# Kernel optimization log

Hardware: AMD Instinct MI355X
Metric: run time of the kernel (lower is better)

Reference implementation:

```python
import jax, jax.numpy as jnp
import numpy as np

DIM = 512
N_HEAD = 4
WIN = (5, 9)

def setup_inputs() -> dict:
    key = jax.random.key(0)
    ks = jax.random.split(key, 9)
    s = DIM ** -0.5
    x = jax.random.normal(ks[0], (1, 8, 60, 108, DIM), jnp.float32)
    Wq = jax.random.normal(ks[1], (DIM, DIM), jnp.float32) * s
    bq = jax.random.normal(ks[2], (DIM,), jnp.float32) * 0.02
    Wk = jax.random.normal(ks[3], (DIM, DIM), jnp.float32) * s
    bk = jax.random.normal(ks[4], (DIM,), jnp.float32) * 0.02
    Wv = jax.random.normal(ks[5], (DIM, DIM), jnp.float32) * s
    bv = jax.random.normal(ks[6], (DIM,), jnp.float32) * 0.02
    Wp = jax.random.normal(ks[7], (DIM, DIM), jnp.float32) * s
    bp = jax.random.normal(ks[8], (DIM,), jnp.float32) * 0.02
    return {"x": x, "Wq": Wq, "bq": bq, "Wk": Wk, "bk": bk,
            "Wv": Wv, "bv": bv, "Wp": Wp, "bp": bp}

def reference(x, Wq, bq, Wk, bk, Wv, bv, Wp, bp):
    b, t, h, w, c = x.shape
    w_h, w_w = WIN
    n_head = N_HEAD
    c_head = c // n_head
    n_wh = -(-h // w_h)
    n_ww = -(-w // w_w)
    new_h, new_w = n_wh * w_h, n_ww * w_w
    pad_b, pad_r = new_h - h, new_w - w
    if pad_b > 0 or pad_r > 0:
        x = jnp.pad(x, ((0, 0), (0, 0), (0, pad_b), (0, pad_r), (0, 0)))
    # torch nn.Linear: y = x @ W.T + b, weight shape (out, in)
    q = jnp.einsum('bthwc,dc->bthwd', x, Wq) + bq
    k = jnp.einsum('bthwc,dc->bthwd', x, Wk) + bk
    v = jnp.einsum('bthwc,dc->bthwd', x, Wv) + bv

    def part(z):
        # (b,t,H,W,c) -> (b, n_windows, n_head, t*w_h*w_w, c_head)
        z = z.reshape(b, t, n_wh, w_h, n_ww, w_w, n_head, c_head)
        z = z.transpose(0, 2, 4, 6, 1, 3, 5, 7)
        return z.reshape(b, n_wh * n_ww, n_head, t * w_h * w_w, c_head)

    qw, kw, vw = part(q), part(k), part(v)
    scale = c_head ** -0.5
    # all (batch, window) attentions batched into one einsum (fused form of the torch double loop)
    scores = jnp.einsum('bwnsc,bwnkc->bwnsk', qw, kw) * scale
    attn = jax.nn.softmax(scores, axis=-1)
    out = jnp.einsum('bwnsk,bwnkc->bwnsc', attn, vw)
    # merge windows back: (b,t,new_h,new_w,c)
    out = out.reshape(b, n_wh, n_ww, n_head, t, w_h, w_w, c_head)
    out = out.transpose(0, 4, 1, 5, 2, 6, 3, 7).reshape(b, t, new_h, new_w, c)
    out = out[:, :, :h, :w, :]
    out = jnp.einsum('bthwc,dc->bthwd', out, Wp) + bp
    return out
```

## Files before the change

kernel.cpp:

```cpp
#include <hip/hip_runtime.h>

typedef _Float16 f16;
typedef _Float16 f16x8 __attribute__((ext_vector_type(8)));
typedef _Float16 f16x4 __attribute__((ext_vector_type(4)));
typedef float f32x4 __attribute__((ext_vector_type(4)));
typedef unsigned int u32;
typedef unsigned int u32x4 __attribute__((ext_vector_type(4)));

#define MFMA16(a, b, c) __builtin_amdgcn_mfma_f32_16x16x32_f16(a, b, c, 0, 0, 0)

__device__ __forceinline__ void async_copy16(f16* lds, const f16* g) {
    __builtin_amdgcn_global_load_lds(
        (const __attribute__((address_space(1))) unsigned int*)g,
        (__attribute__((address_space(3))) unsigned int*)lds,
        16, 0, 0);
}

__global__ __launch_bounds__(256) void prep_convert(
    const float* __restrict__ x, f16* __restrict__ xh,
    const float* __restrict__ Wq, const float* __restrict__ Wk,
    const float* __restrict__ Wv, const float* __restrict__ Wp,
    const float* __restrict__ bq, const float* __restrict__ bk,
    const float* __restrict__ bv,
    f16* __restrict__ Wqkv, f16* __restrict__ Wph, float* __restrict__ bqkv,
    int* __restrict__ tokmap)
{
    if (blockIdx.x < 12960) {
        int i = blockIdx.x * 256 + threadIdx.x;
        f32x4 a = *(const f32x4*)(x + (size_t)i * 8);
        f32x4 b = *(const f32x4*)(x + (size_t)i * 8 + 4);
        f16x8 h = { (f16)a[0], (f16)a[1], (f16)a[2], (f16)a[3],
                    (f16)b[0], (f16)b[1], (f16)b[2], (f16)b[3] };
        *(f16x8*)(xh + (size_t)i * 8) = h;
        return;
    }
    int i = (blockIdx.x - 12960) * 256 + threadIdx.x;
    if (i < 786432) {
        int r = i >> 9, c = i & 511;
        const float* src = (r < 512) ? Wq : (r < 1024) ? Wk : Wv;
        Wqkv[i] = (f16)src[(r & 511) * 512 + c];
    } else if (i < 786432 + 262144) {
        int j = i - 786432;
        Wph[j] = (f16)Wp[j];
    } else if (i < 786432 + 262144 + 1536) {
        int j = i - (786432 + 262144);
        bqkv[j] = (j < 512) ? bq[j] : (j < 1024) ? bk[j - 512] : bv[j - 1024];
    } else if (i < 786432 + 262144 + 1536 + 51840) {
        int j = i - (786432 + 262144 + 1536);
        int t_ = j / 6480, rem = j % 6480;
        int hh = rem / 108, ww = rem % 108;
        int win = (hh / 5) * 12 + (ww / 9);
        int s = t_ * 45 + (hh % 5) * 9 + (ww % 9);
        tokmap[j] = win * 1440 + s;
    }
}

__global__ __launch_bounds__(256, 3) void qkv_gemm(
    const f16* __restrict__ Xh, const f16* __restrict__ W,
    const float* __restrict__ bias, const int* __restrict__ tokmap,
    f16* __restrict__ Qp, f16* __restrict__ Kp, f16* __restrict__ Vp)
{
    __shared__ __align__(16) f16 As[3][128 * 32];
    __shared__ __align__(16) f16 Bs[3][128 * 32];
    const int tid = threadIdx.x;
    const int lane = tid & 63, wid = tid >> 6;
    const int g = lane >> 4, l15 = lane & 15;
    const int wr = wid >> 1, wc = wid & 1;

    const int orig = blockIdx.x;
    const int xcd = orig & 7;
    const int wg = (xcd < 4 ? xcd * 608 : 2432 + (xcd - 4) * 607) + (orig >> 3);
    const int bn = wg % 12;
    const int brow = (wg / 12) * 128;

    const f16* Abase = Xh + (size_t)brow * 512;
    const f16* Bbase = W + (size_t)bn * 128 * 512;

    f32x4 acc[4][4] = {};

    #define QKV_STAGE(buf, step)                                              \
        {                                                                     \
            const int k0_ = (step) * 32;                                      \
            _Pragma("unroll")                                                 \
            for (int rr = 0; rr < 2; ++rr) {                                  \
                int idx = rr * 256 + tid;                                     \
                int row = idx >> 2, ch = idx & 3;                             \
                int sch = ch ^ ((row >> 1) & 3);                              \
                async_copy16(&As[buf][idx * 8],                               \
                             Abase + (size_t)row * 512 + k0_ + sch * 8);      \
                async_copy16(&Bs[buf][idx * 8],                               \
                             Bbase + (size_t)row * 512 + k0_ + sch * 8);      \
            }                                                                 \
        }

    QKV_STAGE(0, 0);
    QKV_STAGE(1, 1);

    int cur = 0;
    for (int t = 0; t < 16; ++t) {
        if (t < 15) asm volatile("s_waitcnt vmcnt(4)" ::: "memory");
        else        asm volatile("s_waitcnt vmcnt(0)" ::: "memory");
        __builtin_amdgcn_s_barrier();
        __builtin_amdgcn_sched_barrier(0);
        if (t + 2 < 16) {
            int stg = cur + 2; if (stg >= 3) stg -= 3;
            QKV_STAGE(stg, t + 2);
        }
        f16x8 a[4], b[4];
        #pragma unroll
        for (int m = 0; m < 4; ++m) {
            int arow = wr * 64 + m * 16 + l15;
            int sl = g ^ ((arow >> 1) & 3);
            a[m] = *(const f16x8*)&As[cur][arow * 32 + sl * 8];
        }
        #pragma unroll
        for (int n = 0; n < 4; ++n) {
            int brw = wc * 64 + n * 16 + l15;
            int sl = g ^ ((brw >> 1) & 3);
            b[n] = *(const f16x8*)&Bs[cur][brw * 32 + sl * 8];
        }
        __builtin_amdgcn_s_setprio(1);
        #pragma unroll
        for (int m = 0; m < 4; ++m)
            #pragma unroll
            for (int n = 0; n < 4; ++n)
                acc[m][n] = MFMA16(a[m], b[n], acc[m][n]);
        __builtin_amdgcn_s_setprio(0);
        __builtin_amdgcn_s_barrier();
        cur = (cur == 2) ? 0 : cur + 1;
    }
    #undef QKV_STAGE

    const int which = bn >> 2, head = bn & 3;
    f16* dst = (which == 0) ? Qp : (which == 1) ? Kp : Vp;
    #pragma unroll
    for (int m = 0; m < 4; ++m) {
        #pragma unroll
        for (int j = 0; j < 4; ++j) {
            int gm = brow + wr * 64 + m * 16 + g * 4 + j;
            size_t obase = ((size_t)(tokmap[gm] + head * 360)) * 128;
            #pragma unroll
            for (int n = 0; n < 4; ++n) {
                int cidx = wc * 64 + n * 16 + l15;
                float v = acc[m][n][j] + bias[bn * 128 + cidx];
                dst[obase + cidx] = (f16)v;
            }
        }
    }
}

__global__ __launch_bounds__(256, 2) void attn_kernel(
    const f16* __restrict__ Qp, const f16* __restrict__ Kp,
    const f16* __restrict__ Vp, f16* __restrict__ AO)
{
    __shared__ __align__(128) f16 Kl[2][64 * 128];
    __shared__ __align__(16)  f16 Vt[128 * 76];
    __shared__ __align__(16)  f16 Pl[192 * 68];

    const int tid = threadIdx.x;
    const int lane = tid & 63, wid = tid >> 6;
    const int g = lane >> 4, l15 = lane & 15;
    const int orig = blockIdx.x;
    const int bid = (orig & 7) * 144 + (orig >> 3);
    const int wh = bid >> 1;
    const int half = bid & 1;
    const int win = wh >> 2, head = wh & 3;
    const int base = wh * 46080;
    const int qbase = half * 192 + wid * 48;

    const float SC2 = 0.08838834764831845f * 1.4426950408889634f;

    #define STAGE_K(buf, kt_)                                                 \
        {                                                                     \
            _Pragma("unroll")                                                 \
            for (int it = 0; it < 4; ++it) {                                  \
                int chunk = it * 256 + tid;                                   \
                int krow = chunk >> 4, c = chunk & 15;                        \
                int sc_ = c ^ (krow & 7);                                     \
                async_copy16(&Kl[buf][chunk * 8],                             \
                    Kp + base + (size_t)((kt_) * 64 + krow) * 128 + sc_ * 8); \
            }                                                                 \
        }

    f16x8 qf[3][4];
    #pragma unroll
    for (int qi = 0; qi < 3; ++qi)
        #pragma unroll
        for (int c4 = 0; c4 < 4; ++c4)
            qf[qi][c4] = *(const f16x8*)(Qp + base + (qbase + qi * 16 + l15) * 128 + c4 * 32 + g * 8);

    STAGE_K(0, 0);

    f32x4 o[3][8] = {};
    float l_r[3] = { 0.f, 0.f, 0.f };

    for (int kt = 0; kt < 6; ++kt) {
        const int cb = kt & 1;
        #pragma unroll
        for (int it = 0; it < 2; ++it) {
            int i2 = it * 256 + tid;
            int kb = i2 >> 6;
            int chp = (i2 & 63) * 2;
            const u32* Vb = (const u32*)(Vp + base);
            u32 d[8];
            #pragma unroll
            for (int i = 0; i < 8; ++i) {
                int kg = kt * 64 + kb * 8 + i;
                d[i] = (kg < 360) ? Vb[kg * 64 + (chp >> 1)] : 0u;
            }
            u32x4 lo, hi;
            #pragma unroll
            for (int jj = 0; jj < 4; ++jj) {
                lo[jj] = (d[2 * jj] & 0xffffu) | (d[2 * jj + 1] << 16);
                hi[jj] = (d[2 * jj] >> 16) | (d[2 * jj + 1] & 0xffff0000u);
            }
            *(u32x4*)&Vt[chp * 76 + kb * 8] = lo;
            *(u32x4*)&Vt[(chp + 1) * 76 + kb * 8] = hi;
        }
        __syncthreads();
        if (kt + 1 < 6) STAGE_K(cb ^ 1, kt + 1);

        f32x4 sc[4][3] = {};
        __builtin_amdgcn_s_setprio(1);
        #pragma unroll
        for (int c4 = 0; c4 < 4; ++c4) {
            f16x8 ka[4];
            #pragma unroll
            for (int kf = 0; kf < 4; ++kf) {
                int row = kf * 16 + l15;
                int sl = (c4 * 4 + g) ^ (row & 7);
                ka[kf] = *(const f16x8*)&Kl[cb][row * 128 + sl * 8];
            }
            #pragma unroll
            for (int kf = 0; kf < 4; ++kf)
                #pragma unroll
                for (int qi = 0; qi < 3; ++qi)
                    sc[kf][qi] = MFMA16(ka[kf], qf[qi][c4], sc[kf][qi]);
        }
        __builtin_amdgcn_s_setprio(0);
        if (kt == 5) {
            #pragma unroll
            for (int kf = 0; kf < 4; ++kf)
                #pragma unroll
                for (int j = 0; j < 4; ++j)
                    if (320 + kf * 16 + g * 4 + j >= 360) {
                        #pragma unroll
                        for (int qi = 0; qi < 3; ++qi) sc[kf][qi][j] = -1e30f;
                    }
        }

        #pragma unroll
        for (int qi = 0; qi < 3; ++qi) {
            float psum = 0.f;
            #pragma unroll
            for (int kf = 0; kf < 4; ++kf) {
                f16x4 pv;
                #pragma unroll
                for (int j = 0; j < 4; ++j) {
                    float p = exp2f(sc[kf][qi][j] * SC2);
                    psum += p;
                    pv[j] = (f16)p;
                }
                *(f16x4*)&Pl[(wid * 48 + qi * 16 + l15) * 68 + kf * 16 + g * 4] = pv;
            }
            psum += __shfl_xor(psum, 16);
            psum += __shfl_xor(psum, 32);
            l_r[qi] += psum;
        }

        __builtin_amdgcn_s_setprio(1);
        #pragma unroll
        for (int kc = 0; kc < 2; ++kc) {
            f16x8 pa[3], vb[8];
            #pragma unroll
            for (int qi = 0; qi < 3; ++qi)
                pa[qi] = *(const f16x8*)&Pl[(wid * 48 + qi * 16 + l15) * 68 + kc * 32 + g * 8];
            #pragma unroll
            for (int chf = 0; chf < 8; ++chf)
                vb[chf] = *(const f16x8*)&Vt[(chf * 16 + l15) * 76 + kc * 32 + g * 8];
            #pragma unroll
            for (int qi = 0; qi < 3; ++qi)
                #pragma unroll
                for (int chf = 0; chf < 8; ++chf)
                    o[qi][chf] = MFMA16(pa[qi], vb[chf], o[qi][chf]);
        }
        __builtin_amdgcn_s_setprio(0);
        __syncthreads();
    }
    #undef STAGE_K

    #pragma unroll
    for (int qi = 0; qi < 3; ++qi) {
        #pragma unroll
        for (int j = 0; j < 4; ++j) {
            float lj = __shfl(l_r[qi], g * 4 + j);
            float inv = 1.0f / lj;
            int s = qbase + qi * 16 + g * 4 + j;
            if (s < 360) {
                int t_ = s / 45, s45 = s % 45;
                int hh = (win / 12) * 5 + s45 / 9;
                int ww = (win % 12) * 9 + s45 % 9;
                int mm = t_ * 6480 + hh * 108 + ww;
                #pragma unroll
                for (int chf = 0; chf < 8; ++chf) {
                    int col = head * 128 + chf * 16 + l15;
                    AO[(size_t)mm * 512 + col] = (f16)(o[qi][chf][j] * inv);
                }
            }
        }
    }
}

__global__ __launch_bounds__(256, 3) void proj_gemm(
    const f16* __restrict__ A, const f16* __restrict__ W,
    const float* __restrict__ bias, float* __restrict__ out)
{
    __shared__ __align__(16) f16 As[3][128 * 32];
    __shared__ __align__(16) f16 Bs[3][128 * 32];
    const int tid = threadIdx.x;
    const int lane = tid & 63, wid = tid >> 6;
    const int g = lane >> 4, l15 = lane & 15;
    const int wr = wid >> 1, wc = wid & 1;

    const int orig = blockIdx.x;
    const int xcd = orig & 7;
    const int wg = (xcd < 4 ? xcd * 203 : 812 + (xcd - 4) * 202) + (orig >> 3);
    const int bcol = (wg & 3) * 128;
    const int brow = (wg >> 2) * 128;

    const f16* Abase = A + (size_t)brow * 512;
    const f16* Bbase = W + (size_t)bcol * 512;

    f32x4 acc[4][4] = {};

    #define PROJ_STAGE(buf, step)                                             \
        {                                                                     \
            const int k0_ = (step) * 32;                                      \
            _Pragma("unroll")                                                 \
            for (int rr = 0; rr < 2; ++rr) {                                  \
                int idx = rr * 256 + tid;                                     \
                int row = idx >> 2, ch = idx & 3;                             \
                int sch = ch ^ ((row >> 1) & 3);                              \
                async_copy16(&As[buf][idx * 8],                               \
                             Abase + (size_t)row * 512 + k0_ + sch * 8);      \
                async_copy16(&Bs[buf][idx * 8],                               \
                             Bbase + (size_t)row * 512 + k0_ + sch * 8);      \
            }                                                                 \
        }

    PROJ_STAGE(0, 0);
    PROJ_STAGE(1, 1);

    int cur = 0;
    for (int t = 0; t < 16; ++t) {
        if (t < 15) asm volatile("s_waitcnt vmcnt(4)" ::: "memory");
        else        asm volatile("s_waitcnt vmcnt(0)" ::: "memory");
        __builtin_amdgcn_s_barrier();
        __builtin_amdgcn_sched_barrier(0);
        if (t + 2 < 16) {
            int stg = cur + 2; if (stg >= 3) stg -= 3;
            PROJ_STAGE(stg, t + 2);
        }
        f16x8 a[4], b[4];
        #pragma unroll
        for (int m = 0; m < 4; ++m) {
            int arow = wr * 64 + m * 16 + l15;
            int sl = g ^ ((arow >> 1) & 3);
            a[m] = *(const f16x8*)&As[cur][arow * 32 + sl * 8];
        }
        #pragma unroll
        for (int n = 0; n < 4; ++n) {
            int brw = wc * 64 + n * 16 + l15;
            int sl = g ^ ((brw >> 1) & 3);
            b[n] = *(const f16x8*)&Bs[cur][brw * 32 + sl * 8];
        }
        __builtin_amdgcn_s_setprio(1);
        #pragma unroll
        for (int m = 0; m < 4; ++m)
            #pragma unroll
            for (int n = 0; n < 4; ++n)
                acc[m][n] = MFMA16(a[m], b[n], acc[m][n]);
        __builtin_amdgcn_s_setprio(0);
        __builtin_amdgcn_s_barrier();
        cur = (cur == 2) ? 0 : cur + 1;
    }
    #undef PROJ_STAGE

    #pragma unroll
    for (int m = 0; m < 4; ++m)
        #pragma unroll
        for (int j = 0; j < 4; ++j) {
            int gm = brow + wr * 64 + m * 16 + g * 4 + j;
            #pragma unroll
            for (int n = 0; n < 4; ++n) {
                int gn = bcol + wc * 64 + n * 16 + l15;
                out[(size_t)gm * 512 + gn] = acc[m][n][j] + bias[gn];
            }
        }
}

extern "C" void kernel_launch(void* const* d_in, const int* in_sizes, int n_in,
                              void* d_out, int out_size, void* d_ws, size_t ws_size,
                              hipStream_t stream)
{
    (void)in_sizes; (void)n_in; (void)out_size; (void)ws_size;
    const float* x  = (const float*)d_in[0];
    const float* Wq = (const float*)d_in[1];
    const float* bq = (const float*)d_in[2];
    const float* Wk = (const float*)d_in[3];
    const float* bk = (const float*)d_in[4];
    const float* Wv = (const float*)d_in[5];
    const float* bv = (const float*)d_in[6];
    const float* Wp = (const float*)d_in[7];
    const float* bp = (const float*)d_in[8];

    f16* Qp   = (f16*)d_ws;
    f16* Kp   = Qp + 26542080;
    f16* Vp   = Kp + 26542080;
    f16* AO   = Vp + 26542080;
    f16* xh   = AO;
    f16* Wqkv = AO + 26542080;
    f16* Wph  = Wqkv + 786432;
    float* bqkv = (float*)(Wph + 262144);
    int* tokmap = (int*)(bqkv + 1536);

    prep_convert<<<17265, 256, 0, stream>>>(x, xh, Wq, Wk, Wv, Wp, bq, bk, bv,
                                            Wqkv, Wph, bqkv, tokmap);
    qkv_gemm<<<4860, 256, 0, stream>>>(xh, Wqkv, bqkv, tokmap, Qp, Kp, Vp);
    attn_kernel<<<1152, 256, 0, stream>>>(Qp, Kp, Vp, AO);
    proj_gemm<<<1620, 256, 0, stream>>>(AO, Wph, bp, (float*)d_out);
}
```

Baseline: 262.3 us.

## Fuse fp32-to-fp16 activation conversion into QKV GEMM with register-staged A loads

Removes the separate pass that converted x to fp16 in a workspace buffer. The QKV GEMM now reads fp32 x directly into registers, converts to fp16 and writes it swizzled into LDS, while B keeps using async global-to-LDS copies. The main loop is restructured into a register double-buffered pipeline with explicit waitcnt/barrier placement. This saves a full write and read of the fp16 copy, but each GEMM block now reads fp32 A 12 times across the N tiles, and register pressure rises.

Result: slower. 305.5 us (+16.5%).

```diff
diff --git a/kernel.cpp b/kernel.cpp
--- a/kernel.cpp
+++ b/kernel.cpp
@@ -16,8 +16,7 @@
         16, 0, 0);
 }
 
-__global__ __launch_bounds__(256) void prep_convert(
-    const float* __restrict__ x, f16* __restrict__ xh,
+__global__ __launch_bounds__(256) void prep_kernel(
     const float* __restrict__ Wq, const float* __restrict__ Wk,
     const float* __restrict__ Wv, const float* __restrict__ Wp,
     const float* __restrict__ bq, const float* __restrict__ bk,
@@ -25,16 +24,7 @@
     f16* __restrict__ Wqkv, f16* __restrict__ Wph, float* __restrict__ bqkv,
     int* __restrict__ tokmap)
 {
-    if (blockIdx.x < 12960) {
-        int i = blockIdx.x * 256 + threadIdx.x;
-        f32x4 a = *(const f32x4*)(x + (size_t)i * 8);
-        f32x4 b = *(const f32x4*)(x + (size_t)i * 8 + 4);
-        f16x8 h = { (f16)a[0], (f16)a[1], (f16)a[2], (f16)a[3],
-                    (f16)b[0], (f16)b[1], (f16)b[2], (f16)b[3] };
-        *(f16x8*)(xh + (size_t)i * 8) = h;
-        return;
-    }
-    int i = (blockIdx.x - 12960) * 256 + threadIdx.x;
+    int i = blockIdx.x * 256 + threadIdx.x;
     if (i < 786432) {
         int r = i >> 9, c = i & 511;
         const float* src = (r < 512) ? Wq : (r < 1024) ? Wk : Wv;
@@ -56,7 +46,7 @@
 }
 
 __global__ __launch_bounds__(256, 3) void qkv_gemm(
-    const f16* __restrict__ Xh, const f16* __restrict__ W,
+    const float* __restrict__ X, const f16* __restrict__ W,
     const float* __restrict__ bias, const int* __restrict__ tokmap,
     f16* __restrict__ Qp, f16* __restrict__ Kp, f16* __restrict__ Vp)
 {
@@ -73,12 +63,37 @@
     const int bn = wg % 12;
     const int brow = (wg / 12) * 128;
 
-    const f16* Abase = Xh + (size_t)brow * 512;
+    const float* Abase = X + (size_t)brow * 512;
     const f16* Bbase = W + (size_t)bn * 128 * 512;
 
     f32x4 acc[4][4] = {};
-
-    #define QKV_STAGE(buf, step)                                              \
+    f32x4 arA[4], arB[4];
+
+    #define LOAD_A(bank, step)                                                \
+        {                                                                     \
+            _Pragma("unroll")                                                 \
+            for (int rr = 0; rr < 4; ++rr) {                                  \
+                int idx = rr * 256 + tid;                                     \
+                int row = idx >> 3, s = idx & 7;                              \
+                bank[rr] = *(const f32x4*)(Abase + (size_t)row * 512 +        \
+                                           (step) * 32 + s * 4);              \
+            }                                                                 \
+        }
+
+    #define CVT_WRITE(bank, step)                                             \
+        {                                                                     \
+            _Pragma("unroll")                                                 \
+            for (int rr = 0; rr < 4; ++rr) {                                  \
+                int idx = rr * 256 + tid;                                     \
+                int row = idx >> 3, s = idx & 7;                              \
+                int ws = (s >> 1) ^ ((row >> 1) & 3);                         \
+                f32x4 v = bank[rr];                                           \
+                f16x4 h = { (f16)v[0], (f16)v[1], (f16)v[2], (f16)v[3] };     \
+                *(f16x4*)&As[(step) % 3][row * 32 + ws * 8 + (s & 1) * 4] = h;\
+            }                                                                 \
+        }
+
+    #define LOAD_B(step)                                                      \
         {                                                                     \
             const int k0_ = (step) * 32;                                      \
             _Pragma("unroll")                                                 \
@@ -86,50 +101,58 @@
                 int idx = rr * 256 + tid;                                     \
                 int row = idx >> 2, ch = idx & 3;                             \
                 int sch = ch ^ ((row >> 1) & 3);                              \
-                async_copy16(&As[buf][idx * 8],                               \
-                             Abase + (size_t)row * 512 + k0_ + sch * 8);      \
-                async_copy16(&Bs[buf][idx * 8],                               \
+                async_copy16(&Bs[(step) % 3][idx * 8],                        \
                              Bbase + (size_t)row * 512 + k0_ + sch * 8);      \
             }                                                                 \
         }
 
-    QKV_STAGE(0, 0);
-    QKV_STAGE(1, 1);
-
-    int cur = 0;
-    for (int t = 0; t < 16; ++t) {
-        if (t < 15) asm volatile("s_waitcnt vmcnt(4)" ::: "memory");
-        else        asm volatile("s_waitcnt vmcnt(0)" ::: "memory");
-        __builtin_amdgcn_s_barrier();
-        __builtin_amdgcn_sched_barrier(0);
-        if (t + 2 < 16) {
-            int stg = cur + 2; if (stg >= 3) stg -= 3;
-            QKV_STAGE(stg, t + 2);
-        }
-        f16x8 a[4], b[4];
-        #pragma unroll
-        for (int m = 0; m < 4; ++m) {
-            int arow = wr * 64 + m * 16 + l15;
-            int sl = g ^ ((arow >> 1) & 3);
-            a[m] = *(const f16x8*)&As[cur][arow * 32 + sl * 8];
-        }
-        #pragma unroll
-        for (int n = 0; n < 4; ++n) {
-            int brw = wc * 64 + n * 16 + l15;
-            int sl = g ^ ((brw >> 1) & 3);
-            b[n] = *(const f16x8*)&Bs[cur][brw * 32 + sl * 8];
-        }
-        __builtin_amdgcn_s_setprio(1);
-        #pragma unroll
-        for (int m = 0; m < 4; ++m)
-            #pragma unroll
-            for (int n = 0; n < 4; ++n)
-                acc[m][n] = MFMA16(a[m], b[n], acc[m][n]);
-        __builtin_amdgcn_s_setprio(0);
-        __builtin_amdgcn_s_barrier();
-        cur = (cur == 2) ? 0 : cur + 1;
-    }
-    #undef QKV_STAGE
+    #define GEMM_STEP(t_, BCUR, BNXT)                                         \
+        {                                                                     \
+            const int cur = (t_) % 3;                                         \
+            f16x8 a[4], b[4];                                                 \
+            _Pragma("unroll")                                                 \
+            for (int m = 0; m < 4; ++m) {                                     \
+                int arow = wr * 64 + m * 16 + l15;                            \
+                int sl = g ^ ((arow >> 1) & 3);                               \
+                a[m] = *(const f16x8*)&As[cur][arow * 32 + sl * 8];           \
+            }                                                                 \
+            _Pragma("unroll")                                                 \
+            for (int n = 0; n < 4; ++n) {                                     \
+                int brw = wc * 64 + n * 16 + l15;                             \
+                int sl = g ^ ((brw >> 1) & 3);                                \
+                b[n] = *(const f16x8*)&Bs[cur][brw * 32 + sl * 8];            \
+            }                                                                 \
+            if ((t_) + 2 < 16) { LOAD_A(BCUR, (t_) + 2); LOAD_B((t_) + 2); }  \
+            if ((t_) + 1 < 16) { CVT_WRITE(BNXT, (t_) + 1); }                 \
+            __builtin_amdgcn_s_setprio(1);                                    \
+            _Pragma("unroll")                                                 \
+            for (int m = 0; m < 4; ++m)                                       \
+                _Pragma("unroll")                                             \
+                for (int n = 0; n < 4; ++n)                                   \
+                    acc[m][n] = MFMA16(a[m], b[n], acc[m][n]);                \
+            __builtin_amdgcn_s_setprio(0);                                    \
+            if ((t_) < 14)                                                    \
+                asm volatile("s_waitcnt vmcnt(6) lgkmcnt(0)" ::: "memory");   \
+            else if ((t_) == 14)                                              \
+                asm volatile("s_waitcnt vmcnt(0) lgkmcnt(0)" ::: "memory");   \
+            if ((t_) < 15) __builtin_amdgcn_s_barrier();                      \
+        }
+
+    LOAD_A(arA, 0); LOAD_B(0);
+    LOAD_A(arB, 1); LOAD_B(1);
+    CVT_WRITE(arA, 0);
+    asm volatile("s_waitcnt vmcnt(6) lgkmcnt(0)" ::: "memory");
+    __builtin_amdgcn_s_barrier();
+
+    #pragma unroll
+    for (int tt = 0; tt < 8; ++tt) {
+        GEMM_STEP(2 * tt,     arA, arB);
+        GEMM_STEP(2 * tt + 1, arB, arA);
+    }
+    #undef GEMM_STEP
+    #undef LOAD_B
+    #undef CVT_WRITE
+    #undef LOAD_A
 
     const int which = bn >> 2, head = bn & 3;
     f16* dst = (which == 0) ? Qp : (which == 1) ? Kp : Vp;
@@ -418,15 +441,14 @@
     f16* Kp   = Qp + 26542080;
     f16* Vp   = Kp + 26542080;
     f16* AO   = Vp + 26542080;
-    f16* xh   = AO;
     f16* Wqkv = AO + 26542080;
     f16* Wph  = Wqkv + 786432;
     float* bqkv = (float*)(Wph + 262144);
     int* tokmap = (int*)(bqkv + 1536);
 
-    prep_convert<<<17265, 256, 0, stream>>>(x, xh, Wq, Wk, Wv, Wp, bq, bk, bv,
-                                            Wqkv, Wph, bqkv, tokmap);
-    qkv_gemm<<<4860, 256, 0, stream>>>(xh, Wqkv, bqkv, tokmap, Qp, Kp, Vp);
+    prep_kernel<<<4305, 256, 0, stream>>>(Wq, Wk, Wv, Wp, bq, bk, bv,
+                                          Wqkv, Wph, bqkv, tokmap);
+    qkv_gemm<<<4860, 256, 0, stream>>>(x, Wqkv, bqkv, tokmap, Qp, Kp, Vp);
     attn_kernel<<<1152, 256, 0, stream>>>(Qp, Kp, Vp, AO);
     proj_gemm<<<1620, 256, 0, stream>>>(AO, Wph, bp, (float*)d_out);
 }
```
